# Optimization experiments

Measured on AMD Instinct MI355X. Metric: run time of the kernel, lower is better.

## Reference

```python
import jax, jax.numpy as jnp
import numpy as np

B, C, H, W = 4, 64, 64, 64
INTER = 16  # in_c // k


def setup_inputs() -> dict:
    key = jax.random.key(0)
    ks = jax.random.split(key, 12)
    sC = 1.0 / np.sqrt(C)
    sI = 1.0 / np.sqrt(INTER)
    return {
        "x":   jax.random.normal(ks[0], (B, C, H, W), dtype=jnp.float32),
        "Wq":  jax.random.normal(ks[1], (INTER, C), dtype=jnp.float32) * sC,
        "bq":  jax.random.normal(ks[2], (INTER,), dtype=jnp.float32) * 0.1,
        "Wk":  jax.random.normal(ks[3], (INTER, C), dtype=jnp.float32) * sC,
        "bk":  jax.random.normal(ks[4], (INTER,), dtype=jnp.float32) * 0.1,
        "wcq": jax.random.normal(ks[5], (INTER,), dtype=jnp.float32) * sI,
        "wck": jax.random.normal(ks[6], (INTER,), dtype=jnp.float32) * sI,
        "Wv":  jax.random.normal(ks[7], (C, C), dtype=jnp.float32) * sC,
        "bv":  jax.random.normal(ks[8], (C,), dtype=jnp.float32) * 0.1,
        "Wg":  jax.random.normal(ks[9], (C, C), dtype=jnp.float32) * sC,
        "bg":  jax.random.normal(ks[10], (C,), dtype=jnp.float32) * 0.1,
    }


def reference(x, Wq, bq, Wk, bk, wcq, wck, Wv, bv, Wg, bg):
    b_, c_, h_, w_ = x.shape
    n = h_ * w_
    xf = x.reshape(b_, c_, n)  # (B, C, N)
    # 1x1 conv projections (per-pixel linear maps)
    q = jnp.einsum('oc,bcn->bon', Wq, xf) + bq[None, :, None]  # (B, inter, N)
    k = jnp.einsum('oc,bcn->bon', Wk, xf) + bk[None, :, None]  # (B, inter, N)
    # concat_conv (1x1, no bias) over [q_i ; k_j] decomposes into an outer sum:
    # energy[b,i,j] = wcq . q[b,:,i] + wck . k[b,:,j]
    a = jnp.einsum('o,bon->bn', wcq, q)  # (B, N)
    d = jnp.einsum('o,bon->bn', wck, k)  # (B, N)
    energy = jax.nn.elu(a[:, :, None] + d[:, None, :])  # (B, N, N)
    energy = energy / (1.5 * jnp.sum(energy, axis=1, keepdims=True))
    v = jnp.einsum('oc,bcn->bon', Wv, xf) + bv[None, :, None]  # (B, C, N)
    out = jnp.einsum('bci,bij->bcj', v, energy)  # (B, C, N)
    # gamma 1x1 conv
    out = jnp.einsum('oc,bcn->bon', Wg, out) + bg[None, :, None]
    return out.reshape(b_, c_, h_, w_)
```

## Files before the change

### kernel.cpp

```cpp
#include <hip/hip_runtime.h>
#include <math.h>

#define NB 4096

#define LEAFo  0
#define MASTo  768
#define RELo   864
#define GHo    1120
#define MEMSET_BYTES 70016
#define VGo    17504
#define ASo    1066080
#define PERMo  1082464
#define Po     1098848
#define PSEAo  1148000
#define PSAo   1148256

__device__ __forceinline__ void gst(float* p, float v) {
    __hip_atomic_store(p, v, __ATOMIC_RELAXED, __HIP_MEMORY_SCOPE_AGENT);
}
__device__ __forceinline__ void gsti(int* p, int v) {
    __hip_atomic_store(p, v, __ATOMIC_RELAXED, __HIP_MEMORY_SCOPE_AGENT);
}

__device__ __forceinline__ int bucket_of(float v) {
    int k = (int)((v + 16.0f) * 128.0f);
    k = k < 0 ? 0 : k;
    k = k > (NB - 1) ? (NB - 1) : k;
    return k;
}

__device__ __forceinline__ void gbar(int* wsi, int idx) {
    __syncthreads();
    if (threadIdx.x == 0) {
        int leaf = blockIdx.x & 7;
        bool bcast = false;
        int old = __hip_atomic_fetch_add(wsi + LEAFo + (idx * 8 + leaf) * 32, 1,
                                         __ATOMIC_RELAXED, __HIP_MEMORY_SCOPE_AGENT);
        if (old == 31) {
            int m = __hip_atomic_fetch_add(wsi + MASTo + idx * 32, 1,
                                           __ATOMIC_RELAXED, __HIP_MEMORY_SCOPE_AGENT);
            if (m == 7) {
#pragma unroll
                for (int i = 0; i < 8; i++)
                    __hip_atomic_store(wsi + RELo + i * 32, idx + 1,
                                       __ATOMIC_RELAXED, __HIP_MEMORY_SCOPE_AGENT);
                bcast = true;
            }
        }
        if (!bcast) {
            const int* myrel = wsi + RELo + leaf * 32;
            while (__hip_atomic_load(myrel, __ATOMIC_RELAXED, __HIP_MEMORY_SCOPE_AGENT) <= idx)
                __builtin_amdgcn_s_sleep(1);
        }
    }
    __syncthreads();
}

__global__ __launch_bounds__(256, 1) void k_fused(
        const float* __restrict__ x,
        const float* __restrict__ Wq, const float* __restrict__ bq,
        const float* __restrict__ Wk, const float* __restrict__ bk,
        const float* __restrict__ wcq, const float* __restrict__ wck,
        const float* __restrict__ Wv, const float* __restrict__ bv,
        const float* __restrict__ Wg, const float* __restrict__ bg,
        float* __restrict__ ws, float* __restrict__ out) {
    __shared__ float smem[13824];
    int tid = threadIdx.x;
    int bid = blockIdx.x;
    int b = bid >> 6, t6 = bid & 63;
    int* wsi = (int*)ws;

    float myA = 0.f, myD = 0.f;
    int   myQ = 0;

    {
        float* xt  = smem;
        float* wt  = smem + 4608;
        float* wgT = smem + 9216;
        float* wqe = smem + 13312, *wke = smem + 13376, *bvg = smem + 13440, *misc = smem + 13504;
        const float4* xb4 = (const float4*)(x + (size_t)b * 64 * 4096);
        float4 xr[4];
#pragma unroll
        for (int k = 0; k < 4; k++) {
            int idx = tid + k * 256, c = idx >> 4, nl4 = idx & 15;
            xr[k] = xb4[c * 1024 + t6 * 16 + nl4];
        }
        {
            const float4* wg4 = (const float4*)Wg;
            int o = tid >> 2;
#pragma unroll
            for (int k4 = 0; k4 < 4; k4++) {
                float4 g = wg4[tid * 4 + k4];
                int m0 = (tid & 3) * 16 + k4 * 4;
                wgT[(m0 + 0) * 64 + o] = g.x; wgT[(m0 + 1) * 64 + o] = g.y;
                wgT[(m0 + 2) * 64 + o] = g.z; wgT[(m0 + 3) * 64 + o] = g.w;
            }
        }
        if (tid < 64) {
            float s1 = 0.f, s2 = 0.f, s3 = 0.f;
            for (int o = 0; o < 16; o++) { s1 += wcq[o] * Wq[o * 64 + tid]; s2 += wck[o] * Wk[o * 64 + tid]; }
            for (int m = 0; m < 64; m++) s3 += Wg[tid * 64 + m] * bv[m];
            wqe[tid] = s1; wke[tid] = s2; bvg[tid] = s3;
        } else if (tid == 64) {
            float s = 0.f; for (int o = 0; o < 16; o++) s += wcq[o] * bq[o]; misc[0] = s;
        } else if (tid == 65) {
            float s = 0.f; for (int o = 0; o < 16; o++) s += wck[o] * bk[o]; misc[1] = s;
        }
#pragma unroll
        for (int k = 0; k < 4; k++) {
            int idx = tid + k * 256, c = idx >> 4, nl4 = idx & 15;
            *(float4*)&xt[c * 72 + nl4 * 4] = xr[k];
        }
        __syncthreads();
        {
            int o = tid & 63, c0 = (tid >> 6) * 16;
            float acc[16];
#pragma unroll
            for (int k = 0; k < 16; k++) acc[k] = 0.f;
            for (int m = 0; m < 64; m++) {
                float wg = wgT[m * 64 + o];
                const float4* wv4 = (const float4*)(Wv + m * 64 + c0);
                float4 a0 = wv4[0], a1 = wv4[1], a2 = wv4[2], a3 = wv4[3];
                acc[0] += wg * a0.x; acc[1] += wg * a0.y; acc[2] += wg * a0.z; acc[3] += wg * a0.w;
                acc[4] += wg * a1.x; acc[5] += wg * a1.y; acc[6] += wg * a1.z; acc[7] += wg * a1.w;
                acc[8] += wg * a2.x; acc[9] += wg * a2.y; acc[10] += wg * a2.z; acc[11] += wg * a2.w;
                acc[12] += wg * a3.x; acc[13] += wg * a3.y; acc[14] += wg * a3.z; acc[15] += wg * a3.w;
            }
#pragma unroll
            for (int k = 0; k < 16; k++) wt[(c0 + k) * 72 + o] = acc[k];
        }
        __syncthreads();
        if (tid < 64) {
            float s1 = misc[0], s2 = misc[1];
            for (int c = 0; c < 64; c++) {
                float xv = xt[c * 72 + tid];
                s1 += wqe[c] * xv; s2 += wke[c] * xv;
            }
            myA = s1; myD = s2;
            atomicAdd(&wsi[GHo + b * 4096 + bucket_of(s1)], 1);
        }
        {
            int o = tid & 63, nl0 = (tid >> 6) * 16;
            float acc[16];
            float bo = bvg[o];
#pragma unroll
            for (int k = 0; k < 16; k++) acc[k] = bo;
            for (int c = 0; c < 64; c++) {
                float wv = wt[c * 72 + o];
                const float* xr2 = &xt[c * 72 + nl0];
#pragma unroll
                for (int k = 0; k < 16; k++) acc[k] += wv * xr2[k];
            }
#pragma unroll
            for (int k = 0; k < 16; k++)
                gst(&ws[VGo + ((size_t)(b * 4096) + t6 * 64 + nl0 + k) * 64 + o], acc[k]);
        }
    }
    gbar(wsi, 0);

    {
        unsigned int* hist = (unsigned int*)smem;
        unsigned int* wtot = hist + 4096;
        int* gh_b = wsi + GHo + b * 4096;
#pragma unroll 4
        for (int i = tid; i < NB; i += 256) hist[i] = (unsigned int)gh_b[i] & 0xFFFFu;
        __syncthreads();
        int lane = tid & 63, w = tid >> 6;
        unsigned int s = 0u; int base = tid * 16;
#pragma unroll
        for (int k = 0; k < 16; k++) s += hist[base + k];
        unsigned int inc = s;
        for (int off = 1; off < 64; off <<= 1) {
            unsigned int u = __shfl_up(inc, off);
            if (lane >= off) inc += u;
        }
        if (lane == 63) wtot[w] = inc;
        __syncthreads();
        unsigned int run = inc - s;
        for (int w2 = 0; w2 < w; w2++) run += wtot[w2];
        for (int k = 0; k < 16; k++) {
            unsigned int h = hist[base + k];
            hist[base + k] = run;
            run += h;
        }
        __syncthreads();
        if (tid < 64) {
            myQ = ((int)hist[bucket_of(-myD)] + 32) >> 6;
            int i = t6 * 64 + tid;
            int kb = bucket_of(myA);
            int old = atomicAdd(&gh_b[kb], 0x10000);
            int r = (int)hist[kb] + (old >> 16);
            gst(&ws[ASo + b * 4096 + r], myA);
            gsti((int*)ws + PERMo + b * 4096 + r, i);
        }
    }
    gbar(wsi, 1);

    {
        int c = tid & 63, w = tid >> 6;
        int r0 = t6 * 64 + w * 16;
        const int* perm = (const int*)ws + PERMo;
        int pk[16]; float avs[16], wvs[16];
#pragma unroll
        for (int k = 0; k < 16; k++) pk[k] = perm[b * 4096 + r0 + k];
#pragma unroll
        for (int k = 0; k < 16; k++) avs[k] = ws[ASo + b * 4096 + r0 + k];
#pragma unroll
        for (int k = 0; k < 16; k++) wvs[k] = ws[VGo + ((size_t)(b * 4096) + pk[k]) * 64 + c];
        float s1 = 0.f, s2 = 0.f, s3 = 0.f, sea_w = 0.f, sa_w = 0.f;
#pragma unroll
        for (int k = 0; k < 16; k++) {
            float ea = expf(avs[k]);
            s1 += wvs[k]; s2 += wvs[k] * ea; s3 += wvs[k] * avs[k];
            sea_w += ea; sa_w += avs[k];
        }
        float* partL = smem;
        float* wsc   = smem + 768;
        partL[(w * 3 + 0) * 64 + c] = s1;
        partL[(w * 3 + 1) * 64 + c] = s2;
        partL[(w * 3 + 2) * 64 + c] = s3;
        if (c == 0) { wsc[w] = sea_w; wsc[4 + w] = sa_w; }
        __syncthreads();
        if (tid < 192) {
            int g = tid >> 6, cc = tid & 63;
            float s = partL[(0 * 3 + g) * 64 + cc] + partL[(1 * 3 + g) * 64 + cc]
                    + partL[(2 * 3 + g) * 64 + cc] + partL[(3 * 3 + g) * 64 + cc];
            gst(&ws[Po + (b * 64 + t6) * 192 + tid], s);
        } else if (tid == 192) {
            gst(&ws[PSEAo + b * 64 + t6], wsc[0] + wsc[1] + wsc[2] + wsc[3]);
        } else if (tid == 193) {
            gst(&ws[PSAo + b * 64 + t6], wsc[4] + wsc[5] + wsc[6] + wsc[7]);
        }
    }
    gbar(wsi, 2);

    {
        float* CP     = smem;
        float* cpsea  = smem + 12545;
        float* cpsa   = smem + 12610;
        float* djs    = smem + 12675;
        float* edjs   = smem + 12739;
        float* invden = smem + 12803;
        int*   qarr   = (int*)(smem + 12867);
        float* bgs    = smem + 12931;
        if (tid < 192) {
            float v[64];
#pragma unroll
            for (int ch = 0; ch < 64; ch++) v[ch] = ws[Po + b * 12288 + ch * 192 + tid];
            float r = 0.f;
#pragma unroll
            for (int q = 0; q < 64; q++) { CP[q * 193 + tid] = r; r += v[q]; }
            CP[64 * 193 + tid] = r;
        } else if (tid == 192) {
            float v[64];
#pragma unroll
            for (int ch = 0; ch < 64; ch++) v[ch] = ws[PSEAo + b * 64 + ch];
            float r = 0.f;
#pragma unroll
            for (int q = 0; q < 64; q++) { cpsea[q] = r; r += v[q]; }
            cpsea[64] = r;
        } else if (tid == 193) {
            float v[64];
#pragma unroll
            for (int ch = 0; ch < 64; ch++) v[ch] = ws[PSAo + b * 64 + ch];
            float r = 0.f;
#pragma unroll
            for (int q = 0; q < 64; q++) { cpsa[q] = r; r += v[q]; }
            cpsa[64] = r;
        }
        if (tid < 64) bgs[tid] = bg[tid];
        __syncthreads();
        int j0 = t6 * 64;
        if (tid < 64) {
            float dj = myD;
            float edj = expf(dj);
            int q = myQ;
            float den = 1.5f * ((cpsa[64] - cpsa[q]) + dj * (float)(4096 - 64 * q)
                                - (float)(64 * q) + edj * cpsea[q]);
            qarr[tid] = q; djs[tid] = dj; edjs[tid] = edj; invden[tid] = 1.0f / den;
        }
        __syncthreads();
        {
            int jl = tid & 63, cq = tid >> 6;
            float dj = djs[jl], edj = edjs[jl], inv = invden[jl];
            int qb = qarr[jl] * 193;
            for (int cc = cq; cc < 64; cc += 4) {
                float c1 = CP[qb + cc], c2 = CP[qb + 64 + cc], c3 = CP[qb + 128 + cc];
                float t1 = CP[64 * 193 + cc], t3 = CP[64 * 193 + 128 + cc];
                float num = (t3 - c3) + dj * t1 - (1.0f + dj) * c1 + edj * c2;
                out[((size_t)(b * 64 + cc)) * 4096 + j0 + jl] = num * inv + bgs[cc];
            }
        }
    }
}

extern "C" void kernel_launch(void* const* d_in, const int* in_sizes, int n_in,
                              void* d_out, int out_size, void* d_ws, size_t ws_size,
                              hipStream_t stream) {
    const float* x   = (const float*)d_in[0];
    const float* Wq  = (const float*)d_in[1];
    const float* bq  = (const float*)d_in[2];
    const float* Wk  = (const float*)d_in[3];
    const float* bk  = (const float*)d_in[4];
    const float* wcq = (const float*)d_in[5];
    const float* wck = (const float*)d_in[6];
    const float* Wv  = (const float*)d_in[7];
    const float* bv  = (const float*)d_in[8];
    const float* Wg  = (const float*)d_in[9];
    const float* bg  = (const float*)d_in[10];
    float* ws  = (float*)d_ws;
    float* out = (float*)d_out;

    hipMemsetAsync(d_ws, 0, MEMSET_BYTES, stream);
    k_fused<<<256, 256, 0, stream>>>(x, Wq, bq, Wk, bk, wcq, wck, Wv, bv, Wg, bg, ws, out);
}
```

Before: 103.3 us.

## Quadruple block size to 1024 threads and split per-thread work across phases

Raises the fused persistent kernel from 256 to 1024 threads per block and cuts per-thread work in every phase from 16 items to 4. The Wg transpose gets a padded stride of 65 to avoid LDS bank conflicts, and the bias fold for bvg now reads from LDS. The aim is more waves per CU to hide latency in the projection, scan, gather and output phases. In exchange, the partial-sum reductions grow to 16 waves, and register pressure and barrier cost rise with 1024-thread blocks.

```diff
diff --git a/kernel.cpp b/kernel.cpp
--- a/kernel.cpp
+++ b/kernel.cpp
@@ -56,7 +56,7 @@
     __syncthreads();
 }
 
-__global__ __launch_bounds__(256, 1) void k_fused(
+__global__ __launch_bounds__(1024, 1) void k_fused(
         const float* __restrict__ x,
         const float* __restrict__ Wq, const float* __restrict__ bq,
         const float* __restrict__ Wk, const float* __restrict__ bk,
@@ -77,57 +77,52 @@
         float* xt  = smem;
         float* wt  = smem + 4608;
         float* wgT = smem + 9216;
-        float* wqe = smem + 13312, *wke = smem + 13376, *bvg = smem + 13440, *misc = smem + 13504;
+        float* wqe = smem + 13376, *wke = smem + 13440, *bvg = smem + 13504, *misc = smem + 13568;
         const float4* xb4 = (const float4*)(x + (size_t)b * 64 * 4096);
-        float4 xr[4];
-#pragma unroll
-        for (int k = 0; k < 4; k++) {
-            int idx = tid + k * 256, c = idx >> 4, nl4 = idx & 15;
-            xr[k] = xb4[c * 1024 + t6 * 16 + nl4];
+        float4 xr;
+        {
+            int c = tid >> 4, nl4 = tid & 15;
+            xr = xb4[c * 1024 + t6 * 16 + nl4];
         }
         {
             const float4* wg4 = (const float4*)Wg;
-            int o = tid >> 2;
-#pragma unroll
-            for (int k4 = 0; k4 < 4; k4++) {
-                float4 g = wg4[tid * 4 + k4];
-                int m0 = (tid & 3) * 16 + k4 * 4;
-                wgT[(m0 + 0) * 64 + o] = g.x; wgT[(m0 + 1) * 64 + o] = g.y;
-                wgT[(m0 + 2) * 64 + o] = g.z; wgT[(m0 + 3) * 64 + o] = g.w;
-            }
-        }
-        if (tid < 64) {
-            float s1 = 0.f, s2 = 0.f, s3 = 0.f;
+            int o = tid >> 4, q4 = tid & 15;
+            float4 g = wg4[tid];
+            int m0 = q4 * 4;
+            wgT[(m0 + 0) * 65 + o] = g.x; wgT[(m0 + 1) * 65 + o] = g.y;
+            wgT[(m0 + 2) * 65 + o] = g.z; wgT[(m0 + 3) * 65 + o] = g.w;
+        }
+        if (tid < 64) {
+            float s1 = 0.f, s2 = 0.f;
             for (int o = 0; o < 16; o++) { s1 += wcq[o] * Wq[o * 64 + tid]; s2 += wck[o] * Wk[o * 64 + tid]; }
-            for (int m = 0; m < 64; m++) s3 += Wg[tid * 64 + m] * bv[m];
-            wqe[tid] = s1; wke[tid] = s2; bvg[tid] = s3;
+            wqe[tid] = s1; wke[tid] = s2;
         } else if (tid == 64) {
             float s = 0.f; for (int o = 0; o < 16; o++) s += wcq[o] * bq[o]; misc[0] = s;
         } else if (tid == 65) {
             float s = 0.f; for (int o = 0; o < 16; o++) s += wck[o] * bk[o]; misc[1] = s;
         }
-#pragma unroll
-        for (int k = 0; k < 4; k++) {
-            int idx = tid + k * 256, c = idx >> 4, nl4 = idx & 15;
-            *(float4*)&xt[c * 72 + nl4 * 4] = xr[k];
-        }
-        __syncthreads();
-        {
-            int o = tid & 63, c0 = (tid >> 6) * 16;
-            float acc[16];
-#pragma unroll
-            for (int k = 0; k < 16; k++) acc[k] = 0.f;
+        {
+            int c = tid >> 4, nl4 = tid & 15;
+            *(float4*)&xt[c * 72 + nl4 * 4] = xr;
+        }
+        __syncthreads();
+        {
+            int o = tid & 63, c0 = (tid >> 6) * 4;
+            float acc[4];
+#pragma unroll
+            for (int k = 0; k < 4; k++) acc[k] = 0.f;
             for (int m = 0; m < 64; m++) {
-                float wg = wgT[m * 64 + o];
-                const float4* wv4 = (const float4*)(Wv + m * 64 + c0);
-                float4 a0 = wv4[0], a1 = wv4[1], a2 = wv4[2], a3 = wv4[3];
+                float wg = wgT[m * 65 + o];
+                float4 a0 = *(const float4*)(Wv + m * 64 + c0);
                 acc[0] += wg * a0.x; acc[1] += wg * a0.y; acc[2] += wg * a0.z; acc[3] += wg * a0.w;
-                acc[4] += wg * a1.x; acc[5] += wg * a1.y; acc[6] += wg * a1.z; acc[7] += wg * a1.w;
-                acc[8] += wg * a2.x; acc[9] += wg * a2.y; acc[10] += wg * a2.z; acc[11] += wg * a2.w;
-                acc[12] += wg * a3.x; acc[13] += wg * a3.y; acc[14] += wg * a3.z; acc[15] += wg * a3.w;
-            }
-#pragma unroll
-            for (int k = 0; k < 16; k++) wt[(c0 + k) * 72 + o] = acc[k];
+            }
+#pragma unroll
+            for (int k = 0; k < 4; k++) wt[(c0 + k) * 72 + o] = acc[k];
+        }
+        if (tid < 64) {
+            float s3 = 0.f;
+            for (int m = 0; m < 64; m++) s3 += wgT[m * 65 + tid] * bv[m];
+            bvg[tid] = s3;
         }
         __syncthreads();
         if (tid < 64) {
@@ -140,19 +135,19 @@
             atomicAdd(&wsi[GHo + b * 4096 + bucket_of(s1)], 1);
         }
         {
-            int o = tid & 63, nl0 = (tid >> 6) * 16;
-            float acc[16];
+            int o = tid & 63, nl0 = (tid >> 6) * 4;
+            float acc[4];
             float bo = bvg[o];
 #pragma unroll
-            for (int k = 0; k < 16; k++) acc[k] = bo;
+            for (int k = 0; k < 4; k++) acc[k] = bo;
             for (int c = 0; c < 64; c++) {
                 float wv = wt[c * 72 + o];
                 const float* xr2 = &xt[c * 72 + nl0];
 #pragma unroll
-                for (int k = 0; k < 16; k++) acc[k] += wv * xr2[k];
-            }
-#pragma unroll
-            for (int k = 0; k < 16; k++)
+                for (int k = 0; k < 4; k++) acc[k] += wv * xr2[k];
+            }
+#pragma unroll
+            for (int k = 0; k < 4; k++)
                 gst(&ws[VGo + ((size_t)(b * 4096) + t6 * 64 + nl0 + k) * 64 + o], acc[k]);
         }
     }
@@ -163,12 +158,12 @@
         unsigned int* wtot = hist + 4096;
         int* gh_b = wsi + GHo + b * 4096;
 #pragma unroll 4
-        for (int i = tid; i < NB; i += 256) hist[i] = (unsigned int)gh_b[i] & 0xFFFFu;
+        for (int i = tid; i < NB; i += 1024) hist[i] = (unsigned int)gh_b[i] & 0xFFFFu;
         __syncthreads();
         int lane = tid & 63, w = tid >> 6;
-        unsigned int s = 0u; int base = tid * 16;
-#pragma unroll
-        for (int k = 0; k < 16; k++) s += hist[base + k];
+        unsigned int s = 0u; int base = tid * 4;
+#pragma unroll
+        for (int k = 0; k < 4; k++) s += hist[base + k];
         unsigned int inc = s;
         for (int off = 1; off < 64; off <<= 1) {
             unsigned int u = __shfl_up(inc, off);
@@ -178,7 +173,7 @@
         __syncthreads();
         unsigned int run = inc - s;
         for (int w2 = 0; w2 < w; w2++) run += wtot[w2];
-        for (int k = 0; k < 16; k++) {
+        for (int k = 0; k < 4; k++) {
             unsigned int h = hist[base + k];
             hist[base + k] = run;
             run += h;
@@ -198,38 +193,45 @@
 
     {
         int c = tid & 63, w = tid >> 6;
-        int r0 = t6 * 64 + w * 16;
+        int r0 = t6 * 64 + w * 4;
         const int* perm = (const int*)ws + PERMo;
-        int pk[16]; float avs[16], wvs[16];
-#pragma unroll
-        for (int k = 0; k < 16; k++) pk[k] = perm[b * 4096 + r0 + k];
-#pragma unroll
-        for (int k = 0; k < 16; k++) avs[k] = ws[ASo + b * 4096 + r0 + k];
-#pragma unroll
-        for (int k = 0; k < 16; k++) wvs[k] = ws[VGo + ((size_t)(b * 4096) + pk[k]) * 64 + c];
+        int pk[4]; float avs[4], wvs[4];
+#pragma unroll
+        for (int k = 0; k < 4; k++) pk[k] = perm[b * 4096 + r0 + k];
+#pragma unroll
+        for (int k = 0; k < 4; k++) avs[k] = ws[ASo + b * 4096 + r0 + k];
+#pragma unroll
+        for (int k = 0; k < 4; k++) wvs[k] = ws[VGo + ((size_t)(b * 4096) + pk[k]) * 64 + c];
         float s1 = 0.f, s2 = 0.f, s3 = 0.f, sea_w = 0.f, sa_w = 0.f;
 #pragma unroll
-        for (int k = 0; k < 16; k++) {
+        for (int k = 0; k < 4; k++) {
             float ea = expf(avs[k]);
             s1 += wvs[k]; s2 += wvs[k] * ea; s3 += wvs[k] * avs[k];
             sea_w += ea; sa_w += avs[k];
         }
         float* partL = smem;
-        float* wsc   = smem + 768;
+        float* wsc   = smem + 3072;
         partL[(w * 3 + 0) * 64 + c] = s1;
         partL[(w * 3 + 1) * 64 + c] = s2;
         partL[(w * 3 + 2) * 64 + c] = s3;
-        if (c == 0) { wsc[w] = sea_w; wsc[4 + w] = sa_w; }
+        if (c == 0) { wsc[w] = sea_w; wsc[16 + w] = sa_w; }
         __syncthreads();
         if (tid < 192) {
             int g = tid >> 6, cc = tid & 63;
-            float s = partL[(0 * 3 + g) * 64 + cc] + partL[(1 * 3 + g) * 64 + cc]
-                    + partL[(2 * 3 + g) * 64 + cc] + partL[(3 * 3 + g) * 64 + cc];
-            gst(&ws[Po + (b * 64 + t6) * 192 + tid], s);
+            float sum = 0.f;
+#pragma unroll
+            for (int ww = 0; ww < 16; ww++) sum += partL[(ww * 3 + g) * 64 + cc];
+            gst(&ws[Po + (b * 64 + t6) * 192 + tid], sum);
         } else if (tid == 192) {
-            gst(&ws[PSEAo + b * 64 + t6], wsc[0] + wsc[1] + wsc[2] + wsc[3]);
+            float sum = 0.f;
+#pragma unroll
+            for (int ww = 0; ww < 16; ww++) sum += wsc[ww];
+            gst(&ws[PSEAo + b * 64 + t6], sum);
         } else if (tid == 193) {
-            gst(&ws[PSAo + b * 64 + t6], wsc[4] + wsc[5] + wsc[6] + wsc[7]);
+            float sum = 0.f;
+#pragma unroll
+            for (int ww = 0; ww < 16; ww++) sum += wsc[16 + ww];
+            gst(&ws[PSAo + b * 64 + t6], sum);
         }
     }
     gbar(wsi, 2);
@@ -284,7 +286,8 @@
             int jl = tid & 63, cq = tid >> 6;
             float dj = djs[jl], edj = edjs[jl], inv = invden[jl];
             int qb = qarr[jl] * 193;
-            for (int cc = cq; cc < 64; cc += 4) {
+#pragma unroll
+            for (int cc = cq; cc < 64; cc += 16) {
                 float c1 = CP[qb + cc], c2 = CP[qb + 64 + cc], c3 = CP[qb + 128 + cc];
                 float t1 = CP[64 * 193 + cc], t3 = CP[64 * 193 + 128 + cc];
                 float num = (t3 - c3) + dj * t1 - (1.0f + dj) * c1 + edj * c2;
@@ -312,5 +315,5 @@
     float* out = (float*)d_out;
 
     hipMemsetAsync(d_ws, 0, MEMSET_BYTES, stream);
-    k_fused<<<256, 256, 0, stream>>>(x, Wq, bq, Wk, bk, wcq, wck, Wv, bv, Wg, bg, ws, out);
-}
+    k_fused<<<256, 1024, 0, stream>>>(x, Wq, bq, Wk, bk, wcq, wck, Wv, bv, Wg, bg, ws, out);
+}
```

Measured after the change: 103.2 us. About the same (-0.0%).
